# Kernel optimization log

Measured on AMD Instinct MI355X. Metric: run time of the kernel, lower is better.

## Reference

```python
import jax, jax.numpy as jnp
import numpy as np
from jax import lax

INPUT_DIM = 1024
HIDDEN_DIM = 2048
N, L = 64, 512


def setup_inputs() -> dict:
    key = jax.random.key(0)
    ks = jax.random.split(key, 6)
    X = jax.random.normal(ks[0], (N, L, INPUT_DIM), dtype=jnp.float32)
    H0 = jnp.zeros((N, HIDDEN_DIM), dtype=jnp.float32)
    # G-invariant layer params (DeepSets invariant map): out = w * sum(x) + b, one per gate (i,f,g,o)
    inv_scale = 1.0 / np.sqrt(INPUT_DIM)
    inv_w = jax.random.normal(ks[1], (4, HIDDEN_DIM), dtype=jnp.float32) * inv_scale
    inv_b = jax.random.normal(ks[2], (4, HIDDEN_DIM), dtype=jnp.float32) * inv_scale
    # Linear(hidden, hidden) per gate, torch convention W: (out, in)
    lin_scale = 1.0 / np.sqrt(HIDDEN_DIM)
    lin_W = jax.random.normal(ks[3], (4, HIDDEN_DIM, HIDDEN_DIM), dtype=jnp.float32) * lin_scale
    lin_b = jax.random.normal(ks[4], (4, HIDDEN_DIM), dtype=jnp.float32) * lin_scale
    return {"X": X, "H0": H0, "inv_w": inv_w, "inv_b": inv_b, "lin_W": lin_W, "lin_b": lin_b}


def reference(X, H0, inv_w, inv_b, lin_W, lin_b):
    # X: (N, L, D); H0: (N, H)
    def step(carry, x_t):
        h, c = carry                               # (N, H), (N, H)
        s = jnp.sum(x_t, axis=-1, keepdims=True)   # (N, 1) invariant statistic
        inv = s * inv_w[:, None, :] + inv_b[:, None, :]            # (4, N, H)
        lin = jnp.einsum('nh,gkh->gnk', h, lin_W) + lin_b[:, None, :]  # (4, N, H)
        z = inv + lin
        i = jax.nn.sigmoid(z[0])
        f = jax.nn.sigmoid(z[1])
        g = jnp.tanh(z[2])
        o = jax.nn.sigmoid(z[3])
        c = f * c + i * g
        h = o * jnp.tanh(c)
        return (h, c), None

    Xt = jnp.swapaxes(X, 0, 1)                     # (L, N, D)
    (h, _), _ = lax.scan(step, (H0, jnp.zeros_like(H0)), Xt)
    # original returns swapdims(hidden_state, 0, 1) -> (H, N)
    return h.T
```

## Files before the change

### kernel.cpp

```cpp
#include <hip/hip_runtime.h>
#include <hip/hip_fp16.h>


typedef _Float16 f16x8 __attribute__((ext_vector_type(8)));
typedef float    f32x4 __attribute__((ext_vector_type(4)));
typedef unsigned long long u64;

static __device__ __forceinline__ float fast_sig(float x) {
  return 1.f / (1.f + __expf(-x));
}
static __device__ __forceinline__ float fast_tanh(float x) {
  x = fminf(15.f, fmaxf(-15.f, x));
  const float e = __expf(2.f * x);
  return (e - 1.f) / (e + 1.f);
}

static __device__ __forceinline__ void st_h16(void* p, float v) {
  const unsigned short b = __builtin_bit_cast(unsigned short, (_Float16)v);
  __hip_atomic_store((unsigned short*)p, b, __ATOMIC_RELAXED, __HIP_MEMORY_SCOPE_AGENT);
}
static __device__ __forceinline__ void st_h64(void* p, u64 v) {
  __hip_atomic_store((u64*)p, v, __ATOMIC_RELAXED, __HIP_MEMORY_SCOPE_AGENT);
}

static __device__ __forceinline__ int h_off(int n, int j) {
  return ((n >> 4) << 16) + ((j >> 5) << 10) + ((n & 15) << 6) +
         (((j >> 3) & 3) << 4) + ((j & 7) << 1);
}

__global__ void __launch_bounds__(256) seq_sum_kernel(const float* __restrict__ X,
                                                      float* s_all) {
  const int gw   = (int)((blockIdx.x * blockDim.x + threadIdx.x) >> 6);
  const int lane = threadIdx.x & 63;
  const int n = gw >> 9, t = gw & 511;
  const float4* p = (const float4*)(X + ((size_t)gw << 10));
  float s = 0.f;
#pragma unroll
  for (int i = 0; i < 4; ++i) {
    const float4 v = p[lane + (i << 6)];
    s += (v.x + v.y) + (v.z + v.w);
  }
#pragma unroll
  for (int off = 32; off; off >>= 1) s += __shfl_xor(s, off);
  if (lane == 0) s_all[(t << 6) + n] = s;
}

__global__ void bar_init_kernel(unsigned* bar) {
  bar[threadIdx.x]       = 0u;
  bar[threadIdx.x + 256] = 0u;
  bar[threadIdx.x + 512] = 0u;
  bar[threadIdx.x + 768] = 0u;
}

static __device__ __forceinline__ void grid_barrier2(unsigned* bar, unsigned round,
                                                     int tid, int blk) {
  asm volatile("s_waitcnt vmcnt(0)" ::: "memory");
  __syncthreads();
  if (tid == 0) {
    unsigned* grp  = bar + ((blk & 7) << 5);
    unsigned* root = bar + 512;
    const unsigned old =
        __hip_atomic_fetch_add(grp, 1u, __ATOMIC_RELAXED, __HIP_MEMORY_SCOPE_AGENT);
    if (old == 32u * round - 1u)
      __hip_atomic_fetch_add(root, 1u, __ATOMIC_RELAXED, __HIP_MEMORY_SCOPE_AGENT);
    const unsigned target = 8u * round;
    unsigned guard = 0;
    while (__hip_atomic_load(root, __ATOMIC_RELAXED, __HIP_MEMORY_SCOPE_AGENT) <
           target) {
      __builtin_amdgcn_s_sleep(1);
      if (++guard > (1u << 23)) break;
    }
  }
  __syncthreads();
}

#define LOAD4(d0, d1, d2, d3, addr)                                         \
  asm volatile("global_load_dwordx4 %0, %4, off sc1\n\t"                    \
               "global_load_dwordx4 %1, %4, off offset:1024 sc1\n\t"        \
               "global_load_dwordx4 %2, %4, off offset:2048 sc1\n\t"        \
               "global_load_dwordx4 %3, %4, off offset:3072 sc1"            \
               : "=v"(d0), "=v"(d1), "=v"(d2), "=v"(d3)                     \
               : "v"(addr)                                                  \
               : "memory")

#define WAITG(n, A)                                                         \
  asm volatile("s_waitcnt vmcnt(" #n ")"                                    \
               : "+v"(A[0]), "+v"(A[1]), "+v"(A[2]), "+v"(A[3]),            \
                 "+v"(A[4]), "+v"(A[5]), "+v"(A[6]), "+v"(A[7]),            \
                 "+v"(A[8]), "+v"(A[9]), "+v"(A[10]), "+v"(A[11]),          \
                 "+v"(A[12]), "+v"(A[13]), "+v"(A[14]), "+v"(A[15])         \
               :                                                            \
               : "memory")

#define KMATH(A, bt)                                                        \
  _Pragma("unroll")                                                         \
  for (int i_ = 0; i_ < 16; ++i_) {                                         \
    acc[bt][0] = __builtin_amdgcn_mfma_f32_16x16x32_f16(A[i_], Wr[i_][0],   \
                                                        acc[bt][0], 0, 0, 0); \
    acc[bt][1] = __builtin_amdgcn_mfma_f32_16x16x32_f16(A[i_], Wr[i_][1],   \
                                                        acc[bt][1], 0, 0, 0); \
  }

__global__ void __launch_bounds__(256, 1) ginv_lstm_persist(
    const float* __restrict__ lin_W, const float* __restrict__ inv_w,
    const float* __restrict__ inv_b, const float* __restrict__ lin_b,
    const float* s_all, const float* __restrict__ H0,
    _Float16* hb0, _Float16* hb1, unsigned* bar, float* out) {
  __shared__ float red[12][64][32];
  __shared__ __align__(16) _Float16 hx[64][8];
  const int blk = blockIdx.x;
  const int tid = threadIdx.x;
  _Float16* hbuf[2] = {hb0, hb1};

  const int wave = tid >> 6;
  const int lane = tid & 63;
  const int q    = lane >> 4;
  const int cc   = lane & 15;

  f16x8 Wr[16][2];
#pragma unroll
  for (int ct = 0; ct < 2; ++ct) {
    const int c  = ct * 16 + cc;
    const int kf = c >> 2, g = c & 3;
    const float* wrow =
        lin_W + (((size_t)(g * 2048 + blk * 8 + kf)) << 11) + wave * 512 + q * 8;
#pragma unroll
    for (int kc = 0; kc < 16; ++kc) {
      const float4 va = *(const float4*)(wrow + kc * 32);
      const float4 vb = *(const float4*)(wrow + kc * 32 + 4);
      f16x8 f;
      f[0] = (_Float16)va.x; f[1] = (_Float16)va.y;
      f[2] = (_Float16)va.z; f[3] = (_Float16)va.w;
      f[4] = (_Float16)vb.x; f[5] = (_Float16)vb.y;
      f[6] = (_Float16)vb.z; f[7] = (_Float16)vb.w;
      Wr[kc][ct] = f;
    }
  }

  {
    int i0 = blk * 512 + tid;
    st_h16((char*)hb0 + h_off(i0 >> 11, i0 & 2047), H0[i0]);
    i0 += 256;
    st_h16((char*)hb0 + h_off(i0 >> 11, i0 & 2047), H0[i0]);
  }

  float iw[2][4], ibb[2][4];
#pragma unroll
  for (int kk = 0; kk < 2; ++kk) {
    const int Kg = blk * 8 + wave + (kk << 2);
#pragma unroll
    for (int g = 0; g < 4; ++g) {
      iw[kk][g]  = inv_w[(g << 11) + Kg];
      ibb[kk][g] = inv_b[(g << 11) + Kg] + lin_b[(g << 11) + Kg];
    }
  }

  unsigned round = 1;
  grid_barrier2(bar, round, tid, blk);

  float cst[2] = {0.f, 0.f};

  const int ld_base = (wave << 14) + (cc << 6) + (q << 4);
  const int st_off = ((lane >> 4) << 16) + ((blk >> 2) << 10) + ((lane & 15) << 6) +
                     ((blk & 3) << 4);

  for (int t = 0; t < 512; ++t) {
    const char* hpb = (const char*)hbuf[t & 1] + ld_base;

    const float sv = s_all[(t << 6) + lane];

    f16x8 pa[16], pb[16];

#pragma unroll
    for (int w = 0; w < 4; ++w)
      LOAD4(pa[w * 4], pa[w * 4 + 1], pa[w * 4 + 2], pa[w * 4 + 3],
            hpb + (w << 12));
#pragma unroll
    for (int w = 0; w < 4; ++w)
      LOAD4(pb[w * 4], pb[w * 4 + 1], pb[w * 4 + 2], pb[w * 4 + 3],
            hpb + 65536 + (w << 12));

    f32x4 acc[4][2];
#pragma unroll
    for (int bt = 0; bt < 4; ++bt)
#pragma unroll
      for (int ct = 0; ct < 2; ++ct) acc[bt][ct] = (f32x4){0.f, 0.f, 0.f, 0.f};

    WAITG(16, pa);
    KMATH(pa, 0);
#pragma unroll
    for (int w = 0; w < 4; ++w)
      LOAD4(pa[w * 4], pa[w * 4 + 1], pa[w * 4 + 2], pa[w * 4 + 3],
            hpb + 131072 + (w << 12));
    WAITG(16, pb);
    KMATH(pb, 1);
#pragma unroll
    for (int w = 0; w < 4; ++w)
      LOAD4(pb[w * 4], pb[w * 4 + 1], pb[w * 4 + 2], pb[w * 4 + 3],
            hpb + 196608 + (w << 12));
    WAITG(16, pa);
    KMATH(pa, 2);
    WAITG(0, pb);
    KMATH(pb, 3);

#pragma unroll
    for (int bt = 0; bt < 4; ++bt)
#pragma unroll
      for (int ct = 0; ct < 2; ++ct) {
        const int c = ct * 16 + cc;
#pragma unroll
        for (int v = 0; v < 4; ++v) {
          const int n = bt * 16 + (q << 2) + v;
          red[wave][n][(((c >> 2) ^ (n & 7)) << 2) + (c & 3)] = acc[bt][ct][v];
        }
      }
    __syncthreads();

    float hnew[2];
#pragma unroll
    for (int kk = 0; kk < 2; ++kk) {
      const int kf  = wave + (kk << 2);
      const int off = (kf ^ (lane & 7)) << 2;
      f32x4 zz = *(const f32x4*)&red[0][lane][off];
#pragma unroll
      for (int w = 1; w < 4; ++w) zz += *(const f32x4*)&red[w][lane][off];
      const float zi = zz[0] + sv * iw[kk][0] + ibb[kk][0];
      const float zf = zz[1] + sv * iw[kk][1] + ibb[kk][1];
      const float zg = zz[2] + sv * iw[kk][2] + ibb[kk][2];
      const float zo = zz[3] + sv * iw[kk][3] + ibb[kk][3];
      const float ig = fast_sig(zi);
      const float fg = fast_sig(zf);
      const float gg = fast_tanh(zg);
      const float og = fast_sig(zo);
      const float cn = fg * cst[kk] + ig * gg;
      cst[kk] = cn;
      hnew[kk] = og * fast_tanh(cn);
    }

    hx[lane][wave]     = (_Float16)hnew[0];
    hx[lane][wave + 4] = (_Float16)hnew[1];
    __syncthreads();
    if (t < 511 && tid < 64) {
      union { f16x8 v; u64 w[2]; } u;
      u.v = *(const f16x8*)hx[lane];
      char* dst = (char*)hbuf[(t + 1) & 1] + st_off;
      st_h64(dst, u.w[0]);
      st_h64(dst + 8, u.w[1]);
    }
    ++round;
    grid_barrier2(bar, round, tid, blk);
  }

  if (tid < 64) {
    const f16x8 hv = *(const f16x8*)hx[lane];
#pragma unroll
    for (int f = 0; f < 8; ++f)
      out[((blk * 8 + f) << 6) + lane] = (float)hv[f];
  }
}

extern "C" void kernel_launch(void* const* d_in, const int* in_sizes, int n_in,
                              void* d_out, int out_size, void* d_ws, size_t ws_size,
                              hipStream_t stream) {
  const float* X     = (const float*)d_in[0];
  const float* H0    = (const float*)d_in[1];
  const float* inv_w = (const float*)d_in[2];
  const float* inv_b = (const float*)d_in[3];
  const float* lin_W = (const float*)d_in[4];
  const float* lin_b = (const float*)d_in[5];
  float* out = (float*)d_out;

  const size_t S_BYTES = 512 * 64 * 4;
  const size_t BAR_PAD = 4096;
  const size_t H_BYTES = 64 * 2048 * 2;
  const size_t NEED = S_BYTES + BAR_PAD + 2 * H_BYTES;

  float*    s_all;
  unsigned* bar;
  _Float16* hb[2];
  if (ws_size >= NEED) {
    char* ws = (char*)d_ws;
    s_all = (float*)ws;
    bar   = (unsigned*)(ws + S_BYTES);
    for (int i = 0; i < 2; ++i)
      hb[i] = (_Float16*)(ws + S_BYTES + BAR_PAD + (size_t)i * H_BYTES);
  } else {
    s_all = (float*)d_out;
    char* xt = (char*)d_in[0] + (size_t)64 * 512 * 1024 * 4 -
               (BAR_PAD + 2 * H_BYTES);
    bar = (unsigned*)xt;
    for (int i = 0; i < 2; ++i)
      hb[i] = (_Float16*)(xt + BAR_PAD + (size_t)i * H_BYTES);
  }

  seq_sum_kernel<<<8192, 256, 0, stream>>>(X, s_all);
  bar_init_kernel<<<1, 256, 0, stream>>>(bar);
  ginv_lstm_persist<<<256, 256, 0, stream>>>(lin_W, inv_w, inv_b, lin_b, s_all, H0,
                                             hb[0], hb[1], bar, out);
}
```

Baseline: 4.252 ms.

## Halve persistent grid to 128 blocks, each owning 16 hidden units

The persistent LSTM kernel now runs on 128 workgroups instead of 256. Each block holds twice as many fp16 weight fragments in registers (16 hidden units times 4 gates) and reduces its partial sums per batch tile through a wider swizzled LDS buffer. Fewer blocks means fewer participants in each per-timestep grid barrier and half as many reloads of the shared h vector. The cost is more MFMA work and register pressure per block, and only half the compute units stay busy.

```diff
diff --git a/kernel.cpp b/kernel.cpp
--- a/kernel.cpp
+++ b/kernel.cpp
@@ -61,7 +61,7 @@
     unsigned* root = bar + 512;
     const unsigned old =
         __hip_atomic_fetch_add(grp, 1u, __ATOMIC_RELAXED, __HIP_MEMORY_SCOPE_AGENT);
-    if (old == 32u * round - 1u)
+    if (old == 16u * round - 1u)
       __hip_atomic_fetch_add(root, 1u, __ATOMIC_RELAXED, __HIP_MEMORY_SCOPE_AGENT);
     const unsigned target = 8u * round;
     unsigned guard = 0;
@@ -92,13 +92,28 @@
                :                                                            \
                : "memory")
 
-#define KMATH(A, bt)                                                        \
+#define KMATH(A)                                                            \
   _Pragma("unroll")                                                         \
   for (int i_ = 0; i_ < 16; ++i_) {                                         \
-    acc[bt][0] = __builtin_amdgcn_mfma_f32_16x16x32_f16(A[i_], Wr[i_][0],   \
-                                                        acc[bt][0], 0, 0, 0); \
-    acc[bt][1] = __builtin_amdgcn_mfma_f32_16x16x32_f16(A[i_], Wr[i_][1],   \
-                                                        acc[bt][1], 0, 0, 0); \
+    acc[0] = __builtin_amdgcn_mfma_f32_16x16x32_f16(A[i_], Wr[i_][0],       \
+                                                    acc[0], 0, 0, 0);       \
+    acc[1] = __builtin_amdgcn_mfma_f32_16x16x32_f16(A[i_], Wr[i_][1],       \
+                                                    acc[1], 0, 0, 0);       \
+    acc[2] = __builtin_amdgcn_mfma_f32_16x16x32_f16(A[i_], Wr[i_][2],       \
+                                                    acc[2], 0, 0, 0);       \
+    acc[3] = __builtin_amdgcn_mfma_f32_16x16x32_f16(A[i_], Wr[i_][3],       \
+                                                    acc[3], 0, 0, 0);       \
+  }
+
+#define SCATTER(bt)                                                         \
+  _Pragma("unroll")                                                         \
+  for (int ct_ = 0; ct_ < 4; ++ct_) {                                       \
+    const int kf_ = ct_ * 4 + (cc >> 2);                                    \
+    _Pragma("unroll")                                                       \
+    for (int v_ = 0; v_ < 4; ++v_) {                                        \
+      const int n_ = (bt)*16 + (q << 2) + v_;                               \
+      red[wave][n_][((kf_ ^ (n_ & 15)) << 2) + (cc & 3)] = acc[ct_][v_];    \
+    }                                                                       \
   }
 
 __global__ void __launch_bounds__(256, 1) ginv_lstm_persist(
@@ -106,8 +121,8 @@
     const float* __restrict__ inv_b, const float* __restrict__ lin_b,
     const float* s_all, const float* __restrict__ H0,
     _Float16* hb0, _Float16* hb1, unsigned* bar, float* out) {
-  __shared__ float red[12][64][32];
-  __shared__ __align__(16) _Float16 hx[64][8];
+  __shared__ __align__(16) float red[6][64][64];
+  __shared__ __align__(16) _Float16 hx[64][16];
   const int blk = blockIdx.x;
   const int tid = threadIdx.x;
   _Float16* hbuf[2] = {hb0, hb1};
@@ -117,13 +132,12 @@
   const int q    = lane >> 4;
   const int cc   = lane & 15;
 
-  f16x8 Wr[16][2];
-#pragma unroll
-  for (int ct = 0; ct < 2; ++ct) {
-    const int c  = ct * 16 + cc;
-    const int kf = c >> 2, g = c & 3;
+  f16x8 Wr[16][4];
+#pragma unroll
+  for (int ct = 0; ct < 4; ++ct) {
+    const int kf = ct * 4 + (cc >> 2), g = cc & 3;
     const float* wrow =
-        lin_W + (((size_t)(g * 2048 + blk * 8 + kf)) << 11) + wave * 512 + q * 8;
+        lin_W + (((size_t)(g * 2048 + blk * 16 + kf)) << 11) + wave * 512 + q * 8;
 #pragma unroll
     for (int kc = 0; kc < 16; ++kc) {
       const float4 va = *(const float4*)(wrow + kc * 32);
@@ -137,17 +151,16 @@
     }
   }
 
-  {
-    int i0 = blk * 512 + tid;
-    st_h16((char*)hb0 + h_off(i0 >> 11, i0 & 2047), H0[i0]);
-    i0 += 256;
-    st_h16((char*)hb0 + h_off(i0 >> 11, i0 & 2047), H0[i0]);
-  }
-
-  float iw[2][4], ibb[2][4];
-#pragma unroll
-  for (int kk = 0; kk < 2; ++kk) {
-    const int Kg = blk * 8 + wave + (kk << 2);
+#pragma unroll
+  for (int i = 0; i < 4; ++i) {
+    const int idx = blk * 1024 + i * 256 + tid;
+    st_h16((char*)hb0 + h_off(idx >> 11, idx & 2047), H0[idx]);
+  }
+
+  float iw[4][4], ibb[4][4];
+#pragma unroll
+  for (int kk = 0; kk < 4; ++kk) {
+    const int Kg = blk * 16 + wave + (kk << 2);
 #pragma unroll
     for (int g = 0; g < 4; ++g) {
       iw[kk][g]  = inv_w[(g << 11) + Kg];
@@ -158,11 +171,11 @@
   unsigned round = 1;
   grid_barrier2(bar, round, tid, blk);
 
-  float cst[2] = {0.f, 0.f};
+  float cst[4] = {0.f, 0.f, 0.f, 0.f};
 
   const int ld_base = (wave << 14) + (cc << 6) + (q << 4);
-  const int st_off = ((lane >> 4) << 16) + ((blk >> 2) << 10) + ((lane & 15) << 6) +
-                     ((blk & 3) << 4);
+  const int st_off = ((lane >> 4) << 16) + ((blk >> 1) << 10) + ((lane & 15) << 6) +
+                     ((blk & 1) << 5);
 
   for (int t = 0; t < 512; ++t) {
     const char* hpb = (const char*)hbuf[t & 1] + ld_base;
@@ -170,6 +183,7 @@
     const float sv = s_all[(t << 6) + lane];
 
     f16x8 pa[16], pb[16];
+    f32x4 acc[4];
 
 #pragma unroll
     for (int w = 0; w < 4; ++w)
@@ -180,47 +194,45 @@
       LOAD4(pb[w * 4], pb[w * 4 + 1], pb[w * 4 + 2], pb[w * 4 + 3],
             hpb + 65536 + (w << 12));
 
-    f32x4 acc[4][2];
-#pragma unroll
-    for (int bt = 0; bt < 4; ++bt)
-#pragma unroll
-      for (int ct = 0; ct < 2; ++ct) acc[bt][ct] = (f32x4){0.f, 0.f, 0.f, 0.f};
-
     WAITG(16, pa);
-    KMATH(pa, 0);
+#pragma unroll
+    for (int ct = 0; ct < 4; ++ct) acc[ct] = (f32x4){0.f, 0.f, 0.f, 0.f};
+    KMATH(pa);
 #pragma unroll
     for (int w = 0; w < 4; ++w)
       LOAD4(pa[w * 4], pa[w * 4 + 1], pa[w * 4 + 2], pa[w * 4 + 3],
             hpb + 131072 + (w << 12));
+    SCATTER(0);
+
     WAITG(16, pb);
-    KMATH(pb, 1);
+#pragma unroll
+    for (int ct = 0; ct < 4; ++ct) acc[ct] = (f32x4){0.f, 0.f, 0.f, 0.f};
+    KMATH(pb);
 #pragma unroll
     for (int w = 0; w < 4; ++w)
       LOAD4(pb[w * 4], pb[w * 4 + 1], pb[w * 4 + 2], pb[w * 4 + 3],
             hpb + 196608 + (w << 12));
+    SCATTER(1);
+
     WAITG(16, pa);
-    KMATH(pa, 2);
+#pragma unroll
+    for (int ct = 0; ct < 4; ++ct) acc[ct] = (f32x4){0.f, 0.f, 0.f, 0.f};
+    KMATH(pa);
+    SCATTER(2);
+
     WAITG(0, pb);
-    KMATH(pb, 3);
-
-#pragma unroll
-    for (int bt = 0; bt < 4; ++bt)
-#pragma unroll
-      for (int ct = 0; ct < 2; ++ct) {
-        const int c = ct * 16 + cc;
-#pragma unroll
-        for (int v = 0; v < 4; ++v) {
-          const int n = bt * 16 + (q << 2) + v;
-          red[wave][n][(((c >> 2) ^ (n & 7)) << 2) + (c & 3)] = acc[bt][ct][v];
-        }
-      }
+#pragma unroll
+    for (int ct = 0; ct < 4; ++ct) acc[ct] = (f32x4){0.f, 0.f, 0.f, 0.f};
+    KMATH(pb);
+    SCATTER(3);
+
     __syncthreads();
 
-    float hnew[2];
-#pragma unroll
-    for (int kk = 0; kk < 2; ++kk) {
+    float hnew[4];
+#pragma unroll
+    for (int kk = 0; kk < 4; ++kk) {
       const int kf  = wave + (kk << 2);
-      const int off = (kf ^ (lane & 7)) << 2;
+      const int off = (kf ^ (lane & 15)) << 2;
       f32x4 zz = *(const f32x4*)&red[0][lane][off];
 #pragma unroll
       for (int w = 1; w < 4; ++w) zz += *(const f32x4*)&red[w][lane][off];
@@ -237,25 +249,27 @@
       hnew[kk] = og * fast_tanh(cn);
     }
 
-    hx[lane][wave]     = (_Float16)hnew[0];
-    hx[lane][wave + 4] = (_Float16)hnew[1];
+#pragma unroll
+    for (int kk = 0; kk < 4; ++kk) hx[lane][wave + (kk << 2)] = (_Float16)hnew[kk];
     __syncthreads();
     if (t < 511 && tid < 64) {
-      union { f16x8 v; u64 w[2]; } u;
-      u.v = *(const f16x8*)hx[lane];
+      union { f16x8 v; u64 w[2]; } u0, u1;
+      u0.v = *(const f16x8*)&hx[lane][0];
+      u1.v = *(const f16x8*)&hx[lane][8];
       char* dst = (char*)hbuf[(t + 1) & 1] + st_off;
-      st_h64(dst, u.w[0]);
-      st_h64(dst + 8, u.w[1]);
+      st_h64(dst,      u0.w[0]);
+      st_h64(dst + 8,  u0.w[1]);
+      st_h64(dst + 16, u1.w[0]);
+      st_h64(dst + 24, u1.w[1]);
     }
     ++round;
     grid_barrier2(bar, round, tid, blk);
   }
 
   if (tid < 64) {
-    const f16x8 hv = *(const f16x8*)hx[lane];
-#pragma unroll
-    for (int f = 0; f < 8; ++f)
-      out[((blk * 8 + f) << 6) + lane] = (float)hv[f];
+#pragma unroll
+    for (int f = 0; f < 16; ++f)
+      out[((blk * 16 + f) << 6) + lane] = (float)hx[lane][f];
   }
 }
 
@@ -295,6 +309,6 @@
 
   seq_sum_kernel<<<8192, 256, 0, stream>>>(X, s_all);
   bar_init_kernel<<<1, 256, 0, stream>>>(bar);
-  ginv_lstm_persist<<<256, 256, 0, stream>>>(lin_W, inv_w, inv_b, lin_b, s_all, H0,
+  ginv_lstm_persist<<<128, 256, 0, stream>>>(lin_W, inv_w, inv_b, lin_b, s_all, H0,
                                              hb[0], hb[1], bar, out);
 }
```

New measurement: 6.379 ms. 1.5x slower.
